# Kernel optimization log

Hardware: AMD Instinct MI355X
Metric: run time of the kernel (lower is better)

Reference implementation:

```python
import jax, jax.numpy as jnp
import numpy as np

jax.config.update("jax_enable_x64", True)  # original torch code runs in float64; minors underflow fp32

D = 96   # Nsites
N = 48   # Nparticles


def setup_inputs() -> dict:
    key = jax.random.key(0)
    # Orthonormal single-particle orbitals (columns), as the module assumes (P^T P = I)
    A = jax.random.normal(key, (D, D), dtype=jnp.float64)
    Q, _ = jnp.linalg.qr(A)
    P = Q[:, :N]  # [D, N]
    # A valid ordered particle configuration: strictly increasing, occ_positions[k] <= D-N+k
    occ_positions = jnp.arange(N, dtype=jnp.int32) * (D // N)  # stride-2 filling
    return {"P": P, "occ_positions": occ_positions}


def _cond_probs(P, occ_positions):
    """Conditional probabilities probs[k, x] of placing the k-th (ordered) particle at
    site x given particles 0..k-1 at occ_positions[0..k-1].

    Math identical to SlaterDetSampler_ordered.get_cond_prob (naive_update=True):
      G = I - P P^T
      probs[k,x] = -det(M_x[0:x+1,0:x+1]) / det(M[0:xmin,0:xmin])
    where M = G - diag(occupancy of particles < k) and M_x additionally sets n_x = 1.
    Since Ksites is always the contiguous range 0..x, all determinants are LEADING
    principal minors; and because only the (x,x) diagonal entry changes by -1 (last index
    of the block), det(M_x block) = d_{x+1} - d_x with d_j the leading j-minor of M.
    """
    Dd, Nn = P.shape
    dt = P.dtype
    eye = jnp.eye(Dd, dtype=dt)
    G = eye - P @ P.T                                             # [D, D]

    onehots = jax.nn.one_hot(occ_positions, Dd, dtype=dt)         # [N, D]
    n_before = jnp.cumsum(onehots, axis=0) - onehots              # occupancy of particles < k
    A = G[None] - n_before[:, :, None] * eye                      # [N, D, D]: G - diag(n_<k)

    # All leading principal minors via batched det of masked matrices:
    # M_j = A on the [0:j,0:j] block, identity elsewhere  =>  det(M_j) = leading j-minor
    ii = jnp.arange(Dd)
    jj = jnp.arange(1, Dd + 1)
    blk = (ii[None, :, None] < jj[:, None, None]) & (ii[None, None, :] < jj[:, None, None])  # [D,D,D]
    Ms = jnp.where(blk[None], A[:, None], eye)                    # [N, D, D, D]
    d = jnp.linalg.det(Ms.reshape(Nn * Dd, Dd, Dd)).reshape(Nn, Dd)
    d_full = jnp.concatenate([jnp.ones((Nn, 1), dt), d], axis=1)  # d_full[k, j] = j-th leading minor

    k = jnp.arange(Nn)
    xmin = jnp.where(k == 0, 0, occ_positions[jnp.maximum(k - 1, 0)] + 1)  # [N]
    xmax = Dd - Nn + k + 1                                                  # [N]
    denom = jnp.take_along_axis(d_full, xmin[:, None], axis=1)              # [N, 1]
    num = d_full[:, 1:] - d_full[:, :-1]                                    # det(GG_num) per candidate x

    x = jnp.arange(Dd)
    support = (x[None, :] >= xmin[:, None]) & (x[None, :] < xmax[:, None])
    probs = jnp.where(support, -num / denom, jnp.zeros((), dt))
    # torch.where(abs(probs) > 1e-15, probs, 0.)
    probs = jnp.where(jnp.abs(probs) > 1e-15, probs, jnp.zeros((), dt))
    return probs


def reference(P, occ_positions):
    probs = _cond_probs(P, occ_positions)                          # [N, D]
    # prob of the full ordered sample = prod_k probs[k, occ_positions[k]]  (as in sample())
    p_k = jnp.take_along_axis(probs, occ_positions[:, None], axis=1)[:, 0]
    prob_sample = jnp.prod(p_k)
    return probs, prob_sample
```

## Files before the change

kernel.cpp:

```cpp
#include <hip/hip_runtime.h>
#include <math.h>

#define Dd 96
#define Nn 48
#define LD 97
#define PTS 98

__device__ __forceinline__ double frcp(double x) {
    double r = __builtin_amdgcn_rcp(x);
    r = fma(fma(-x, r, 1.0), r, r);
    r = fma(fma(-x, r, 1.0), r, r);
    return r;
}

__global__ __launch_bounds__(1024, 1) void slater_kernel(const float* __restrict__ P,
                                                         const int* __restrict__ occ,
                                                         float* __restrict__ out,
                                                         unsigned* __restrict__ cnt) {
    __shared__ double As[Dd * LD];
    __shared__ unsigned char flag[Dd];
    float* PT = (float*)As;

    const int tid  = threadIdx.x;
    const int k    = blockIdx.x;
    const int n    = Dd - Nn + k + 1;
    const int lane = tid & 63;
    const int wave = tid >> 6;
    const int xmin = (k == 0) ? 0 : occ[k - 1] + 1;

    if (tid < Dd) flag[tid] = 0;
    __syncthreads();
    if (tid < k) flag[occ[tid]] = 1;
    for (int e = tid; e < Dd * Nn; e += 1024) {
        int c = e / Nn, t = e - (e / Nn) * Nn;
        PT[t * PTS + c] = P[e];
    }
    __syncthreads();

    double Areg[8]; int trs[2], tcs[2];
#pragma unroll
    for (int it = 0; it < 2; ++it) {
        int tau = tid + 1024 * it;
        double s00 = 0.0, s01 = 0.0, s10 = 0.0, s11 = 0.0;
        int tr = 0, tc = 0;
        if (tau < 1176) {
            tr = (int)((97.0 - sqrt(9409.0 - 8.0 * (double)tau)) * 0.5);
            while ((tr * (97 - tr)) / 2 > tau) --tr;
            while (((tr + 1) * (96 - tr)) / 2 <= tau) ++tr;
            tc = tr + (tau - (tr * (97 - tr)) / 2);
            int r0 = 2 * tr, c0 = 2 * tc;
            if (r0 < n && c0 < n) {
                for (int t = 0; t < Nn; ++t) {
                    const float* row = PT + t * PTS;
                    float2 pr = *(const float2*)(row + r0);
                    float2 pc = *(const float2*)(row + c0);
                    s00 -= (double)pr.x * (double)pc.x; s01 -= (double)pr.x * (double)pc.y;
                    s10 -= (double)pr.y * (double)pc.x; s11 -= (double)pr.y * (double)pc.y;
                }
            }
        }
        trs[it] = tr; tcs[it] = tc;
        Areg[it * 4 + 0] = s00; Areg[it * 4 + 1] = s01;
        Areg[it * 4 + 2] = s10; Areg[it * 4 + 3] = s11;
    }
    __syncthreads();
#pragma unroll
    for (int it = 0; it < 2; ++it) {
        int tau = tid + 1024 * it;
        if (tau < 1176) {
            int tr = trs[it], tc = tcs[it];
            int r0 = 2 * tr, c0 = 2 * tc;
            if (r0 < n && c0 < n) {
                bool r1 = (r0 + 1 < n), c1 = (c0 + 1 < n);
                double d0 = flag[r0] ? 0.0 : 1.0;
                double d1 = flag[r0 + 1] ? 0.0 : 1.0;
                As[r0 * LD + c0] = Areg[it * 4 + 0] + ((r0 == c0) ? d0 : 0.0);
                if (c1)       As[r0 * LD + c0 + 1]       = Areg[it * 4 + 1];
                if (r1)       As[(r0 + 1) * LD + c0]     = Areg[it * 4 + 2];
                if (r1 && c1) As[(r0 + 1) * LD + c0 + 1] = Areg[it * 4 + 3] + ((r0 == c0) ? d1 : 0.0);
                if (tr != tc) {
                    As[c0 * LD + r0] = Areg[it * 4 + 0];
                    if (c1)       As[(c0 + 1) * LD + r0]     = Areg[it * 4 + 1];
                    if (r1)       As[c0 * LD + r0 + 1]       = Areg[it * 4 + 2];
                    if (r1 && c1) As[(c0 + 1) * LD + r0 + 1] = Areg[it * 4 + 3];
                }
            }
        }
    }
    __syncthreads();

    double runprod = 1.0;
    double myprob  = 0.0;
    bool   dead    = false;

    auto guard = [&](int jj, double pivot) {
        double ap = fabs(pivot);
        if (jj >= xmin) {
            if (tid == jj) myprob = runprod * (1.0 - pivot);
            double newrun = runprod * pivot;
            if (!(ap > 1e-7) || !(ap < 8.0) || !(fabs(newrun) > 1e-8)) dead = true;
            else runprod = newrun;
        } else {
            if (!(ap > 1e-12) || !(ap < 8.0)) dead = true;
        }
    };

    int j = 0;
    for (; !dead && j + 4 <= n - 1; j += 4) {
        int t = n - (j + 4);
        bool ok0 = (lane < t), ok1 = (lane + 64 < t);
        int c0 = j + 4 + (ok0 ? lane : 0);
        int c1 = j + 4 + (ok1 ? lane + 64 : 0);
        double R0c0 = As[j * LD + c0],       R1c0 = As[(j + 1) * LD + c0];
        double R2c0 = As[(j + 2) * LD + c0], R3c0 = As[(j + 3) * LD + c0];
        double R0c1 = As[j * LD + c1],       R1c1 = As[(j + 1) * LD + c1];
        double R2c1 = As[(j + 2) * LD + c1], R3c1 = As[(j + 3) * LD + c1];

        const double* Bp0 = As + j * LD + j;
        const double* Bp1 = Bp0 + LD;
        const double* Bp2 = Bp1 + LD;
        const double* Bp3 = Bp2 + LD;
        double B00 = Bp0[0], B01 = Bp0[1], B02 = Bp0[2], B03 = Bp0[3];
        double B10 = Bp1[0], B11 = Bp1[1], B12 = Bp1[2], B13 = Bp1[3];
        double B20 = Bp2[0], B21 = Bp2[1], B22 = Bp2[2], B23 = Bp2[3];
        double B30 = Bp3[0], B31 = Bp3[1], B32 = Bp3[2], B33 = Bp3[3];

        double piv0 = B00;
        double rp0  = frcp(piv0);
        double m10  = B10 * rp0;
        double u01 = B01, u02 = B02, u03 = B03;
        double piv1 = B11 - m10 * u01;
        double u12  = B12 - m10 * u02;
        double u13  = B13 - m10 * u03;
        double rp1  = frcp(piv1);
        double m20  = B20 * rp0;
        double m21  = (B21 - m20 * u01) * rp1;
        double piv2 = B22 - m20 * u02 - m21 * u12;
        double u23  = B23 - m20 * u03 - m21 * u13;
        double rp2  = frcp(piv2);
        double m30  = B30 * rp0;
        double m31  = (B31 - m30 * u01) * rp1;
        double m32  = (B32 - m30 * u02 - m31 * u12) * rp2;
        double piv3 = B33 - m30 * u03 - m31 * u13 - m32 * u23;
        double rp3  = frcp(piv3);

        guard(j + 0, piv0);
        if (!dead) guard(j + 1, piv1);
        if (!dead) guard(j + 2, piv2);
        if (!dead) guard(j + 3, piv3);

        if (!dead) {
            double y0 = R0c0;
            double y1 = R1c0 - m10 * y0;
            double y2 = R2c0 - m20 * y0 - m21 * y1;
            double y3 = R3c0 - m30 * y0 - m31 * y1 - m32 * y2;
            double s3c0 = y3 * rp3;
            double s2c0 = (y2 - u23 * s3c0) * rp2;
            double s1c0 = (y1 - u12 * s2c0 - u13 * s3c0) * rp1;
            double s0c0 = (y0 - u01 * s1c0 - u02 * s2c0 - u03 * s3c0) * rp0;
            double z0 = R0c1;
            double z1 = R1c1 - m10 * z0;
            double z2 = R2c1 - m20 * z0 - m21 * z1;
            double z3 = R3c1 - m30 * z0 - m31 * z1 - m32 * z2;
            double s3c1 = z3 * rp3;
            double s2c1 = (z2 - u23 * s3c1) * rp2;
            double s1c1 = (z1 - u12 * s2c1 - u13 * s3c1) * rp1;
            double s0c1 = (z0 - u01 * s1c1 - u02 * s2c1 - u03 * s3c1) * rp0;

            for (int i = j + 4 + wave; i < n; i += 64) {
                double a0[4], a1[4], a2[4], a3[4], T0[4], T1[4];
                bool h[4];
#pragma unroll
                for (int u = 0; u < 4; ++u) {
                    int r = i + u * 16;
                    h[u] = (r < n);
                    const double* rw = As + (h[u] ? r : i) * LD;
                    a0[u] = rw[j];     a1[u] = rw[j + 1];
                    a2[u] = rw[j + 2]; a3[u] = rw[j + 3];
                    T0[u] = rw[c0];    T1[u] = rw[c1];
                }
#pragma unroll
                for (int u = 0; u < 4; ++u) {
                    if (h[u]) {
                        double* rw = As + (i + u * 16) * LD;
                        if (ok0) rw[c0] = T0[u] - a0[u] * s0c0 - a1[u] * s1c0
                                                - a2[u] * s2c0 - a3[u] * s3c0;
                        if (ok1) rw[c1] = T1[u] - a0[u] * s0c1 - a1[u] * s1c1
                                                - a2[u] * s2c1 - a3[u] * s3c1;
                    }
                }
            }
        }
        __syncthreads();
    }

    for (; !dead && j < n - 1; ++j) {
        double pivot = As[j * LD + j];
        guard(j, pivot);
        if (dead) break;
        double rp = frcp(pivot);
        int t = n - 1 - j;
        double r0 = (lane < t)      ? As[j * LD + j + 1 + lane]  : 0.0;
        double r1 = (lane + 64 < t) ? As[j * LD + j + 65 + lane] : 0.0;
        for (int i = j + 1 + wave; i < n; i += 16) {
            double mult = As[i * LD + j] * rp;
            if (lane < t)      As[i * LD + j + 1 + lane]  -= mult * r0;
            if (lane + 64 < t) As[i * LD + j + 65 + lane] -= mult * r1;
        }
        __syncthreads();
    }
    if (!dead && tid == n - 1) {
        double pl = As[(n - 1) * LD + (n - 1)];
        myprob = runprod * (1.0 - pl);
    }

    if (tid < Dd) {
        double p = myprob;
        if (!isfinite(p)) p = 0.0;
        if (!(fabs(p) > 1e-15)) p = 0.0;
        p = fmin(fmax(p, 0.0), 1.0);
        out[k * Dd + tid] = (float)p;
    }

    __threadfence();
    __syncthreads();
    if (wave == 0) {
        int old = 0;
        if (lane == 0)
            old = (int)__hip_atomic_fetch_add(cnt, 1u, __ATOMIC_ACQ_REL,
                                              __HIP_MEMORY_SCOPE_AGENT);
        old = __shfl(old, 0, 64);
        if (((unsigned)old + 1u) % (unsigned)Nn == 0u) {
            __threadfence();
            double v = 1.0;
            if (lane < Nn) {
                float f = __hip_atomic_load(out + lane * Dd + occ[lane],
                                            __ATOMIC_RELAXED, __HIP_MEMORY_SCOPE_AGENT);
                v = (double)f;
            }
#pragma unroll
            for (int off = 32; off >= 1; off >>= 1)
                v *= __shfl_down(v, off, 64);
            if (lane == 0) {
                if (!isfinite(v)) v = 0.0;
                out[Nn * Dd] = (float)v;
            }
        }
    }
}

extern "C" void kernel_launch(void* const* d_in, const int* in_sizes, int n_in,
                              void* d_out, int out_size, void* d_ws, size_t ws_size,
                              hipStream_t stream) {
    const float* P = (const float*)d_in[0];
    const int* occ = (const int*)d_in[1];
    float* out = (float*)d_out;

    slater_kernel<<<Nn, 1024, 0, stream>>>(P, occ, out, (unsigned*)d_ws);
}
```

Baseline: 109.2 us.

## Pipeline 4x4 panel factorization on a dedicated wave with lookahead

Wave 15 now factors the next 4x4 diagonal block as soon as waves 0-3 have updated the first rows of the trailing matrix. Readiness is signalled through an LDS atomic counter, and the factors are double-buffered in shared memory. This takes the serial per-step panel factorization and guard logic off the critical path of the other 15 waves, which now only read the precomputed factors. The cost is that one wave no longer does trailing updates (the row stride drops to 15), plus extra spin-wait and fence synchronization. There is also a risk of subtle ordering bugs in the LDS producer/consumer handoff.

```diff
diff --git a/kernel.cpp b/kernel.cpp
--- a/kernel.cpp
+++ b/kernel.cpp
@@ -18,6 +18,13 @@
                                                          float* __restrict__ out,
                                                          unsigned* __restrict__ cnt) {
     __shared__ double As[Dd * LD];
+    __shared__ double fac[2][16];
+    __shared__ double ev[2][4];
+    __shared__ int    evmask[2];
+    __shared__ int    sdead[2];
+    __shared__ double gs_runprod;
+    __shared__ int    gs_dead;
+    __shared__ int    rdy;
     __shared__ unsigned char flag[Dd];
     float* PT = (float*)As;
 
@@ -28,6 +35,7 @@
     const int wave = tid >> 6;
     const int xmin = (k == 0) ? 0 : occ[k - 1] + 1;
 
+    if (tid == 0) rdy = 0;
     if (tid < Dd) flag[tid] = 0;
     __syncthreads();
     if (tid < k) flag[occ[tid]] = 1;
@@ -89,114 +97,158 @@
     }
     __syncthreads();
 
-    double runprod = 1.0;
-    double myprob  = 0.0;
-    bool   dead    = false;
-
-    auto guard = [&](int jj, double pivot) {
-        double ap = fabs(pivot);
-        if (jj >= xmin) {
-            if (tid == jj) myprob = runprod * (1.0 - pivot);
-            double newrun = runprod * pivot;
-            if (!(ap > 1e-7) || !(ap < 8.0) || !(fabs(newrun) > 1e-8)) dead = true;
-            else runprod = newrun;
+    double myprob = 0.0;
+    double grun = 1.0;
+    int    gdead = 0;
+
+    auto prefactor = [&](int jb, int p) {
+        const double* q0 = As + jb * LD + jb;
+        const double* q1 = q0 + LD;
+        const double* q2 = q1 + LD;
+        const double* q3 = q2 + LD;
+        double B00=q0[0],B01=q0[1],B02=q0[2],B03=q0[3];
+        double B10=q1[0],B11=q1[1],B12=q1[2],B13=q1[3];
+        double B20=q2[0],B21=q2[1],B22=q2[2],B23=q2[3];
+        double B30=q3[0],B31=q3[1],B32=q3[2],B33=q3[3];
+        double piv0=B00, rp0=frcp(piv0);
+        double m10=B10*rp0;
+        double u01=B01,u02=B02,u03=B03;
+        double piv1=B11-m10*u01;
+        double u12=B12-m10*u02, u13=B13-m10*u03;
+        double rp1=frcp(piv1);
+        double m20=B20*rp0;
+        double m21=(B21-m20*u01)*rp1;
+        double piv2=B22-m20*u02-m21*u12;
+        double u23=B23-m20*u03-m21*u13;
+        double rp2=frcp(piv2);
+        double m30=B30*rp0;
+        double m31=(B31-m30*u01)*rp1;
+        double m32=(B32-m30*u02-m31*u12)*rp2;
+        double piv3=B33-m30*u03-m31*u13-m32*u23;
+        double rp3=frcp(piv3);
+        double pivs[4]={piv0,piv1,piv2,piv3};
+        double evv[4]={0.0,0.0,0.0,0.0};
+        int msk=0;
+#pragma unroll
+        for (int q = 0; q < 4; ++q) {
+            if (!gdead) {
+                int jj = jb + q;
+                double piv = pivs[q];
+                double ap = fabs(piv);
+                if (jj >= xmin) {
+                    evv[q] = grun * (1.0 - piv);
+                    msk |= (1 << q);
+                    double nr = grun * piv;
+                    if (!(ap > 1e-7) || !(ap < 8.0) || !(fabs(nr) > 1e-8)) gdead = 1;
+                    else grun = nr;
+                } else {
+                    if (!(ap > 1e-12) || !(ap < 8.0)) gdead = 1;
+                }
+            }
+        }
+        fac[p][0]=m10; fac[p][1]=m20; fac[p][2]=m21; fac[p][3]=m30; fac[p][4]=m31; fac[p][5]=m32;
+        fac[p][6]=u01; fac[p][7]=u02; fac[p][8]=u03; fac[p][9]=u12; fac[p][10]=u13; fac[p][11]=u23;
+        fac[p][12]=rp0; fac[p][13]=rp1; fac[p][14]=rp2; fac[p][15]=rp3;
+        ev[p][0]=evv[0]; ev[p][1]=evv[1]; ev[p][2]=evv[2]; ev[p][3]=evv[3];
+        evmask[p]=msk; sdead[p]=gdead;
+        gs_runprod=grun; gs_dead=gdead;
+    };
+
+    if (wave == 15 && lane == 0) prefactor(0, 0);
+    __syncthreads();
+
+    int j = 0, s = 0, target = 4;
+    for (; j + 4 <= n - 1; j += 4, ++s) {
+        const int par = s & 1;
+        if ((tid >> 2) == s) {
+            int q = tid & 3;
+            if ((evmask[par] >> q) & 1) myprob = ev[par][q];
+        }
+        if (sdead[par]) break;
+        const bool nextex = (j + 8 <= n - 1);
+
+        if (wave == 15) {
+            if (nextex) {
+                while (__hip_atomic_load(&rdy, __ATOMIC_ACQUIRE,
+                                         __HIP_MEMORY_SCOPE_WORKGROUP) < target)
+                    __builtin_amdgcn_s_sleep(1);
+                target += 4;
+                __threadfence_block();
+                if (lane == 0) prefactor(j + 4, par ^ 1);
+            }
         } else {
-            if (!(ap > 1e-12) || !(ap < 8.0)) dead = true;
-        }
-    };
-
-    int j = 0;
-    for (; !dead && j + 4 <= n - 1; j += 4) {
-        int t = n - (j + 4);
-        bool ok0 = (lane < t), ok1 = (lane + 64 < t);
-        int c0 = j + 4 + (ok0 ? lane : 0);
-        int c1 = j + 4 + (ok1 ? lane + 64 : 0);
-        double R0c0 = As[j * LD + c0],       R1c0 = As[(j + 1) * LD + c0];
-        double R2c0 = As[(j + 2) * LD + c0], R3c0 = As[(j + 3) * LD + c0];
-        double R0c1 = As[j * LD + c1],       R1c1 = As[(j + 1) * LD + c1];
-        double R2c1 = As[(j + 2) * LD + c1], R3c1 = As[(j + 3) * LD + c1];
-
-        const double* Bp0 = As + j * LD + j;
-        const double* Bp1 = Bp0 + LD;
-        const double* Bp2 = Bp1 + LD;
-        const double* Bp3 = Bp2 + LD;
-        double B00 = Bp0[0], B01 = Bp0[1], B02 = Bp0[2], B03 = Bp0[3];
-        double B10 = Bp1[0], B11 = Bp1[1], B12 = Bp1[2], B13 = Bp1[3];
-        double B20 = Bp2[0], B21 = Bp2[1], B22 = Bp2[2], B23 = Bp2[3];
-        double B30 = Bp3[0], B31 = Bp3[1], B32 = Bp3[2], B33 = Bp3[3];
-
-        double piv0 = B00;
-        double rp0  = frcp(piv0);
-        double m10  = B10 * rp0;
-        double u01 = B01, u02 = B02, u03 = B03;
-        double piv1 = B11 - m10 * u01;
-        double u12  = B12 - m10 * u02;
-        double u13  = B13 - m10 * u03;
-        double rp1  = frcp(piv1);
-        double m20  = B20 * rp0;
-        double m21  = (B21 - m20 * u01) * rp1;
-        double piv2 = B22 - m20 * u02 - m21 * u12;
-        double u23  = B23 - m20 * u03 - m21 * u13;
-        double rp2  = frcp(piv2);
-        double m30  = B30 * rp0;
-        double m31  = (B31 - m30 * u01) * rp1;
-        double m32  = (B32 - m30 * u02 - m31 * u12) * rp2;
-        double piv3 = B33 - m30 * u03 - m31 * u13 - m32 * u23;
-        double rp3  = frcp(piv3);
-
-        guard(j + 0, piv0);
-        if (!dead) guard(j + 1, piv1);
-        if (!dead) guard(j + 2, piv2);
-        if (!dead) guard(j + 3, piv3);
-
-        if (!dead) {
-            double y0 = R0c0;
-            double y1 = R1c0 - m10 * y0;
-            double y2 = R2c0 - m20 * y0 - m21 * y1;
-            double y3 = R3c0 - m30 * y0 - m31 * y1 - m32 * y2;
-            double s3c0 = y3 * rp3;
-            double s2c0 = (y2 - u23 * s3c0) * rp2;
-            double s1c0 = (y1 - u12 * s2c0 - u13 * s3c0) * rp1;
-            double s0c0 = (y0 - u01 * s1c0 - u02 * s2c0 - u03 * s3c0) * rp0;
-            double z0 = R0c1;
-            double z1 = R1c1 - m10 * z0;
-            double z2 = R2c1 - m20 * z0 - m21 * z1;
-            double z3 = R3c1 - m30 * z0 - m31 * z1 - m32 * z2;
-            double s3c1 = z3 * rp3;
-            double s2c1 = (z2 - u23 * s3c1) * rp2;
-            double s1c1 = (z1 - u12 * s2c1 - u13 * s3c1) * rp1;
-            double s0c1 = (z0 - u01 * s1c1 - u02 * s2c1 - u03 * s3c1) * rp0;
-
-            for (int i = j + 4 + wave; i < n; i += 64) {
-                double a0[4], a1[4], a2[4], a3[4], T0[4], T1[4];
-                bool h[4];
-#pragma unroll
-                for (int u = 0; u < 4; ++u) {
-                    int r = i + u * 16;
-                    h[u] = (r < n);
-                    const double* rw = As + (h[u] ? r : i) * LD;
-                    a0[u] = rw[j];     a1[u] = rw[j + 1];
-                    a2[u] = rw[j + 2]; a3[u] = rw[j + 3];
-                    T0[u] = rw[c0];    T1[u] = rw[c1];
-                }
-#pragma unroll
-                for (int u = 0; u < 4; ++u) {
-                    if (h[u]) {
-                        double* rw = As + (i + u * 16) * LD;
-                        if (ok0) rw[c0] = T0[u] - a0[u] * s0c0 - a1[u] * s1c0
-                                                - a2[u] * s2c0 - a3[u] * s3c0;
-                        if (ok1) rw[c1] = T1[u] - a0[u] * s0c1 - a1[u] * s1c1
-                                                - a2[u] * s2c1 - a3[u] * s3c1;
-                    }
+            const int t = n - (j + 4);
+            const bool ok0 = (lane < t), ok1 = (lane + 64 < t);
+            const int c0 = j + 4 + (ok0 ? lane : 0);
+            const int c1 = j + 4 + (ok1 ? lane + 64 : 0);
+            const double m10=fac[par][0], m20=fac[par][1], m21=fac[par][2],
+                         m30=fac[par][3], m31=fac[par][4], m32=fac[par][5];
+            const double u01=fac[par][6], u02=fac[par][7], u03=fac[par][8],
+                         u12=fac[par][9], u13=fac[par][10], u23=fac[par][11];
+            const double rp0=fac[par][12], rp1=fac[par][13],
+                         rp2=fac[par][14], rp3=fac[par][15];
+            const double R0c0=As[j*LD+c0],     R1c0=As[(j+1)*LD+c0];
+            const double R2c0=As[(j+2)*LD+c0], R3c0=As[(j+3)*LD+c0];
+            const double R0c1=As[j*LD+c1],     R1c1=As[(j+1)*LD+c1];
+            const double R2c1=As[(j+2)*LD+c1], R3c1=As[(j+3)*LD+c1];
+            double y0=R0c0, y1=R1c0-m10*y0, y2=R2c0-m20*y0-m21*y1,
+                   y3=R3c0-m30*y0-m31*y1-m32*y2;
+            double s3c0=y3*rp3, s2c0=(y2-u23*s3c0)*rp2,
+                   s1c0=(y1-u12*s2c0-u13*s3c0)*rp1,
+                   s0c0=(y0-u01*s1c0-u02*s2c0-u03*s3c0)*rp0;
+            double z0=R0c1, z1=R1c1-m10*z0, z2=R2c1-m20*z0-m21*z1,
+                   z3=R3c1-m30*z0-m31*z1-m32*z2;
+            double s3c1=z3*rp3, s2c1=(z2-u23*s3c1)*rp2,
+                   s1c1=(z1-u12*s2c1-u13*s3c1)*rp1,
+                   s0c1=(z0-u01*s1c1-u02*s2c1-u03*s3c1)*rp0;
+
+            int i = j + 4 + wave;
+            if (i < n) {
+                {
+                    double* rw = As + i * LD;
+                    double a0=rw[j], a1=rw[j+1], a2=rw[j+2], a3=rw[j+3];
+                    double T0=rw[c0], T1=rw[c1];
+                    double v0=T0 - a0*s0c0 - a1*s1c0 - a2*s2c0 - a3*s3c0;
+                    double v1=T1 - a0*s0c1 - a1*s1c1 - a2*s2c1 - a3*s3c1;
+                    if (ok0) rw[c0]=v0;
+                    if (ok1) rw[c1]=v1;
+                }
+                if (wave < 4 && nextex) {
+                    __threadfence_block();
+                    if (lane == 0)
+                        __hip_atomic_fetch_add(&rdy, 1, __ATOMIC_RELEASE,
+                                               __HIP_MEMORY_SCOPE_WORKGROUP);
+                }
+                for (i += 15; i < n; i += 15) {
+                    double* rw = As + i * LD;
+                    double a0=rw[j], a1=rw[j+1], a2=rw[j+2], a3=rw[j+3];
+                    double T0=rw[c0], T1=rw[c1];
+                    double v0=T0 - a0*s0c0 - a1*s1c0 - a2*s2c0 - a3*s3c0;
+                    double v1=T1 - a0*s0c1 - a1*s1c1 - a2*s2c1 - a3*s3c1;
+                    if (ok0) rw[c0]=v0;
+                    if (ok1) rw[c1]=v1;
                 }
             }
         }
         __syncthreads();
     }
+
+    double runprod = gs_runprod;
+    bool   dead    = (gs_dead != 0);
 
     for (; !dead && j < n - 1; ++j) {
         double pivot = As[j * LD + j];
-        guard(j, pivot);
+        {
+            double ap = fabs(pivot);
+            if (j >= xmin) {
+                if (tid == j) myprob = runprod * (1.0 - pivot);
+                double nr = runprod * pivot;
+                if (!(ap > 1e-7) || !(ap < 8.0) || !(fabs(nr) > 1e-8)) dead = true;
+                else runprod = nr;
+            } else {
+                if (!(ap > 1e-12) || !(ap < 8.0)) dead = true;
+            }
+        }
         if (dead) break;
         double rp = frcp(pivot);
         int t = n - 1 - j;
```

Result: faster. 105.8 us (-3.1%).
